# Kernel optimization log

Hardware: AMD Instinct MI355X
Metric: run time of the kernel (lower is better)

## Reference

```python
import jax, jax.numpy as jnp
import numpy as np

B, L, DIM = 4, 2048, 512
H, D = 8, 64
SCALE = D ** -0.5
NEG = -10000.0


def setup_inputs() -> dict:
    key = jax.random.key(0)
    ks = jax.random.split(key, 5)
    std = 1.0 / np.sqrt(DIM)
    return {
        "x": jax.random.normal(ks[0], (B, L, DIM), dtype=jnp.float32),
        "wq": jax.random.normal(ks[1], (H * D, DIM), dtype=jnp.float32) * std,
        "wk": jax.random.normal(ks[2], (H * D, DIM), dtype=jnp.float32) * std,
        "wv": jax.random.normal(ks[3], (H * D, DIM), dtype=jnp.float32) * std,
        "wo": jax.random.normal(ks[4], (DIM, H * D), dtype=jnp.float32) * std,
    }


def reference(x, wq, wk, wv, wo):
    b, l, _ = x.shape
    # projections (torch Linear: y = x @ W.T), split heads -> [b,h,l,d]
    q = (x @ wq.T).reshape(b, l, H, D).transpose(0, 2, 1, 3)
    k = (x @ wk.T).reshape(b, l, H, D).transpose(0, 2, 1, 3)
    v = (x @ wv.T).reshape(b, l, H, D).transpose(0, 2, 1, 3)
    scores = jnp.einsum("bhld,bhsd->bhls", q, k) * SCALE
    scores = jnp.nan_to_num(scores, nan=0.0, posinf=10000.0, neginf=NEG)
    diag = jnp.eye(l, dtype=bool)[None, None]  # [1,1,l,l]
    scores = jnp.where(diag, NEG, scores)
    attn = jax.nn.softmax(scores, axis=-1)
    attn = jnp.where(diag, 0.0, attn)
    attn = jnp.nan_to_num(attn, nan=0.0, posinf=0.0, neginf=0.0)
    out = jnp.einsum("bhls,bhsd->bhld", attn, v)
    out = out.transpose(0, 2, 1, 3).reshape(b, l, H * D)
    return out @ wo.T
```

## Files before the change

### kernel.cpp

```cpp
#include <hip/hip_runtime.h>
#include <hip/hip_bf16.h>


#define Bsz 4
#define Lsz 2048
#define DIMsz 512
#define Hsz 8
#define Dsz 64

typedef _Float16 f16;
typedef __attribute__((ext_vector_type(8))) _Float16 f16x8;
typedef __attribute__((ext_vector_type(4))) _Float16 f16x4;
typedef __attribute__((ext_vector_type(2))) __fp16 fp16x2;
typedef __attribute__((ext_vector_type(4))) float f32x4;
typedef __attribute__((ext_vector_type(16))) float f32x16;
typedef unsigned int u32;
typedef __attribute__((ext_vector_type(2))) unsigned int u32x2;

#if __has_builtin(__builtin_amdgcn_exp2f)
#define EXP2(x) __builtin_amdgcn_exp2f(x)
#else
#define EXP2(x) __expf(0.6931471805599453f * (x))
#endif

__device__ __forceinline__ u32 pack2(float a, float b) {
#if __has_builtin(__builtin_amdgcn_cvt_pkrtz)
    fp16x2 h = __builtin_amdgcn_cvt_pkrtz(a, b);
    return __builtin_bit_cast(u32, h);
#else
    fp16x2 h; h.x = (__fp16)a; h.y = (__fp16)b;
    return __builtin_bit_cast(u32, h);
#endif
}

#if __has_builtin(__builtin_amdgcn_permlane32_swap)
__device__ __forceinline__ void plswap(u32& a, u32& b) {
    u32x2 r = __builtin_amdgcn_permlane32_swap(a, b, false, false);
    a = r.x; b = r.y;
}
#else
__device__ __forceinline__ void plswap(u32& a, u32& b) {
    u32 sa = (u32)__shfl_xor((int)a, 32);
    u32 sb = (u32)__shfl_xor((int)b, 32);
    bool hi = (threadIdx.x & 32) != 0;
    u32 na = hi ? sb : a;
    u32 nb = hi ? b : sa;
    a = na; b = nb;
}
#endif

__device__ __forceinline__ void gl2lds16(const void* g, void* l) {
    __builtin_amdgcn_global_load_lds(
        (const __attribute__((address_space(1))) u32*)g,
        (__attribute__((address_space(3))) u32*)l, 16, 0, 0);
}

__global__ __launch_bounds__(256) void pack_f16(
    const float* __restrict__ x, const float* __restrict__ wq,
    const float* __restrict__ wk, const float* __restrict__ wv,
    const float* __restrict__ wo,
    f16* __restrict__ xh, f16* __restrict__ w3h, f16* __restrict__ woh)
{
    int bx = blockIdx.x, seg, blk;
    if (bx < 4096) { seg = 0; blk = bx; }
    else { seg = 1 + ((bx - 4096) >> 8); blk = (bx - 4096) & 255; }
    const float* s; f16* d; float sc = 1.0f;
    switch (seg) {
        case 0: s = x;  d = xh;            break;
        case 1: s = wq; d = w3h;           sc = 0.18033688011112042f; break;
        case 2: s = wk; d = w3h + 262144;  break;
        case 3: s = wv; d = w3h + 524288;  break;
        default: s = wo; d = woh;          break;
    }
    int i = (blk * 256 + threadIdx.x) * 4;
    float4 v = *(const float4*)(s + i);
    f16x4 o;
    o.x = (f16)(v.x * sc); o.y = (f16)(v.y * sc);
    o.z = (f16)(v.z * sc); o.w = (f16)(v.w * sc);
    *(f16x4*)(d + i) = o;
}

__global__ __launch_bounds__(256) void gemm_qkv_f16(
    const f16* __restrict__ A, const f16* __restrict__ B,
    f16* __restrict__ qh, f16* __restrict__ kh, f16* __restrict__ vth)
{
    __shared__ __align__(16) char smem[32768];
    f16* Ash = (f16*)smem;
    f16* Bsh = (f16*)(smem + 16384);

    const int tid = threadIdx.x;
    const int w = tid >> 6, lane = tid & 63;
    const int quad = lane >> 4, low = lane & 15;
    const int wm = w >> 1, wn = w & 1;
    const int m0 = blockIdx.y * 128, n0 = blockIdx.x * 128;

    f32x4 acc[4][4];
    #pragma unroll
    for (int i = 0; i < 4; i++)
        #pragma unroll
        for (int j = 0; j < 4; j++) acc[i][j] = (f32x4){0.f, 0.f, 0.f, 0.f};

    #pragma unroll 1
    for (int k0 = 0; k0 < DIMsz; k0 += 64) {
        __syncthreads();
        #pragma unroll
        for (int j = 0; j < 4; j++) {
            int t = j * 256 + tid;
            int r = t >> 3, g = t & 7;
            int gc = (g ^ (r & 7)) * 8;
            char* lb = (char*)Ash + (j * 256 + w * 64) * 16;
            gl2lds16(A + (size_t)(m0 + r) * DIMsz + k0 + gc, lb);
            char* lb2 = (char*)Bsh + (j * 256 + w * 64) * 16;
            gl2lds16(B + (size_t)(n0 + r) * DIMsz + k0 + gc, lb2);
        }
        __syncthreads();

        #pragma unroll
        for (int ks2 = 0; ks2 < 2; ks2++) {
            f16x8 af[4], bf[4];
            #pragma unroll
            for (int mt = 0; mt < 4; mt++) {
                int ar = wm * 64 + mt * 16 + low;
                int c = ks2 * 4 + quad;
                af[mt] = *(const f16x8*)&Ash[ar * 64 + ((c ^ (ar & 7)) << 3)];
            }
            #pragma unroll
            for (int nt = 0; nt < 4; nt++) {
                int br = wn * 64 + nt * 16 + low;
                int c = ks2 * 4 + quad;
                bf[nt] = *(const f16x8*)&Bsh[br * 64 + ((c ^ (br & 7)) << 3)];
            }
            #pragma unroll
            for (int mt = 0; mt < 4; mt++)
                #pragma unroll
                for (int nt = 0; nt < 4; nt++)
                    acc[mt][nt] = __builtin_amdgcn_mfma_f32_16x16x32_f16(
                        af[mt], bf[nt], acc[mt][nt], 0, 0, 0);
        }
    }

    const int proj = n0 >> 9;
    if (proj < 2) {
        f16* dst = (proj == 0) ? qh : kh;
        #pragma unroll
        for (int nt = 0; nt < 4; nt++) {
            int n = n0 + wn * 64 + nt * 16 + low;
            int c = n & 511, h = c >> 6, d = c & 63;
            #pragma unroll
            for (int mt = 0; mt < 4; mt++)
                #pragma unroll
                for (int r = 0; r < 4; r++) {
                    int m = m0 + wm * 64 + mt * 16 + quad * 4 + r;
                    int b_ = m >> 11, l = m & (Lsz - 1);
                    size_t bh = (size_t)(b_ * Hsz + h);
                    dst[(bh * Lsz + l) * Dsz + d] = (f16)acc[mt][nt][r];
                }
        }
    } else {
        const int hb = (n0 & 511) >> 6;
        f16* Tv = (f16*)smem;
        const int b_ = m0 >> 11, l0 = m0 & (Lsz - 1);
        #pragma unroll 1
        for (int hs = 0; hs < 2; hs++) {
            __syncthreads();
            if (wn == hs) {
                #pragma unroll
                for (int nt = 0; nt < 4; nt++) {
                    int d = nt * 16 + low;
                    #pragma unroll
                    for (int mt = 0; mt < 4; mt++)
                        #pragma unroll
                        for (int r = 0; r < 4; r++) {
                            int l = wm * 64 + mt * 16 + quad * 4 + r;
                            Tv[d * 136 + l] = (f16)acc[mt][nt][r];
                        }
                }
            }
            __syncthreads();
            int d = tid >> 2, seg = tid & 3;
            size_t bh = (size_t)(b_ * Hsz + hb + hs);
            f16* dstp = vth + (bh * 64 + d) * (size_t)Lsz + l0 + seg * 32;
            const f16* srcp = Tv + d * 136 + seg * 32;
            #pragma unroll
            for (int j = 0; j < 4; j++)
                *(f16x8*)(dstp + j * 8) = *(const f16x8*)(srcp + j * 8);
        }
    }
}

__global__ __launch_bounds__(256, 4) void attn_mfma(
    const f16* __restrict__ q, const f16* __restrict__ k,
    const f16* __restrict__ vt, f16* __restrict__ ctx)
{
    __shared__ __align__(16) char smem[33792];

    const int tid = threadIdx.x;
    const int w = tid >> 6, lane = tid & 63;
    const int col = lane & 31;
    const int h = lane >> 5;
    const int kw = w & 1, qw = w >> 1;
    const int bh = blockIdx.x;
    const int qb = blockIdx.y;
    const int q0 = qb * 64;
    const size_t kvb = (size_t)bh * Lsz;

    f16* Ks = (f16*)smem;
    f16* Vs = (f16*)(smem + 16384);

    f16x8 qf[4];
    #pragma unroll
    for (int s = 0; s < 4; s++)
        qf[s] = *(const f16x8*)(q + (kvb + q0 + qw * 32 + col) * Dsz
                                  + s * 16 + h * 8);
    #pragma unroll
    for (int s = 0; s < 4; s++)
        asm volatile("" :: "v"(qf[s]));

    const f16* kp; const f16* vp;
    {
        int r8 = tid >> 3, g8 = tid & 7;
        int gc = (g8 ^ (r8 & 7) ^ ((r8 >> 3) & 3)) << 3;
        kp = k + (kvb + r8) * Dsz + gc;
        vp = vt + ((size_t)bh * Dsz + r8) * Lsz + gc;
    }
    char* kl = (char*)smem + w * 1024;
    char* vl = (char*)smem + 16384 + w * 1024;

    const int cswz = (col & 7) ^ ((col >> 3) & 3);
    const f16* kfp[4];
    #pragma unroll
    for (int s = 0; s < 4; s++)
        kfp[s] = Ks + (kw * 32 + col) * 64 + (((s * 2 + h) ^ cswz) << 3);
    const f16* vfp[2][2];
    #pragma unroll
    for (int dt = 0; dt < 2; dt++)
        #pragma unroll
        for (int ks = 0; ks < 2; ks++) {
            int cv = kw * 4 + ks * 2 + h;
            vfp[dt][ks] = Vs + (dt * 32 + col) * 64 + ((cv ^ cswz) << 3);
        }

    f32x16 acc[2];
    #pragma unroll
    for (int dt = 0; dt < 2; dt++)
        #pragma unroll
        for (int i = 0; i < 16; i++) acc[dt][i] = 0.f;
    float lsum = 0.f;

    gl2lds16(kp,            kl);
    gl2lds16(kp + 32 * Dsz, kl + 4096);
    gl2lds16(vp,            vl);
    gl2lds16(vp + 32 * Lsz, vl + 4096);
    kp += 64 * Dsz;
    vp += 64;

#define ATTN_ROUND(S0, P, PRE) do {                                           \
    const int ko_ = (P) * 8192;                                               \
    if (PRE) {                                                                \
        const int nx_ = ((P) ^ 1) * 8192;                                     \
        gl2lds16(kp,            kl + nx_);                                    \
        gl2lds16(kp + 32 * Dsz, kl + nx_ + 4096);                             \
        gl2lds16(vp,            vl + nx_);                                    \
        gl2lds16(vp + 32 * Lsz, vl + nx_ + 4096);                             \
        kp += 64 * Dsz;                                                       \
        vp += 64;                                                             \
        asm volatile("s_waitcnt vmcnt(4)" ::: "memory");                      \
    } else {                                                                  \
        asm volatile("s_waitcnt vmcnt(0)" ::: "memory");                      \
    }                                                                         \
    __builtin_amdgcn_s_barrier();                                             \
    __builtin_amdgcn_sched_barrier(0);                                        \
      \
    f32x16 st;                                                                \
    _Pragma("unroll")                                                         \
    for (int i = 0; i < 16; i++) st[i] = 0.f;                                 \
    __builtin_amdgcn_s_setprio(1);                                            \
    _Pragma("unroll")                                                         \
    for (int s = 0; s < 4; s++) {                                             \
        f16x8 kf = *(const f16x8*)((const char*)kfp[s] + ko_);                \
        st = __builtin_amdgcn_mfma_f32_32x32x16_f16(kf, qf[s], st, 0, 0, 0);  \
    }                                                                         \
    __builtin_amdgcn_s_setprio(0);                                            \
                \
    _Pragma("unroll")                                                         \
    for (int i = 0; i < 16; i++) st[i] = EXP2(st[i]);                         \
    if ((S0) == q0 && kw == qw) {                                             \
        _Pragma("unroll")                                                     \
        for (int i = 0; i < 16; i++) {                                        \
            int row = (i & 3) + 8 * (i >> 2) + 4 * h;                         \
            st[i] = (row == col) ? 0.f : st[i];                               \
        }                                                                     \
    }                                                                         \
    _Pragma("unroll")                                                         \
    for (int i = 0; i < 16; i++) lsum += st[i];                               \
                                                \
    u32 P2[8];                                                                \
    _Pragma("unroll")                                                         \
    for (int j = 0; j < 8; j++)                                               \
        P2[j] = pack2(st[2 * j], st[2 * j + 1]);                              \
    plswap(P2[0], P2[2]); plswap(P2[1], P2[3]);                               \
    plswap(P2[4], P2[6]); plswap(P2[5], P2[7]);                               \
    union { u32 u[4]; f16x8 v; } pfa, pfb;                                    \
    _Pragma("unroll")                                                         \
    for (int jj = 0; jj < 4; jj++) {                                          \
        pfa.u[jj] = P2[jj];                                                   \
        pfb.u[jj] = P2[4 + jj];                                               \
    }                                                                         \
                               \
    __builtin_amdgcn_s_setprio(1);                                            \
    _Pragma("unroll")                                                         \
    for (int dt = 0; dt < 2; dt++) {                                          \
        f16x8 vf0 = *(const f16x8*)((const char*)vfp[dt][0] + ko_);           \
        acc[dt] = __builtin_amdgcn_mfma_f32_32x32x16_f16(                     \
            vf0, pfa.v, acc[dt], 0, 0, 0);                                    \
        f16x8 vf1 = *(const f16x8*)((const char*)vfp[dt][1] + ko_);           \
        acc[dt] = __builtin_amdgcn_mfma_f32_32x32x16_f16(                     \
            vf1, pfb.v, acc[dt], 0, 0, 0);                                    \
    }                                                                         \
    __builtin_amdgcn_s_setprio(0);                                            \
    __builtin_amdgcn_sched_barrier(0);                                        \
    __builtin_amdgcn_s_barrier();                                             \
} while (0)

    #pragma unroll 1
    for (int s0 = 0; s0 < Lsz; s0 += 128) {
        ATTN_ROUND(s0, 0, true);
        ATTN_ROUND(s0 + 64, 1, (s0 + 128 < Lsz));
    }
#undef ATTN_ROUND

    __syncthreads();

    float* Lsp = (float*)(smem + 32768);
    lsum += __shfl_xor(lsum, 32);
    if (h == 0) Lsp[qw * 64 + kw * 32 + col] = lsum;

    float* Om = (float*)smem;
    if (kw == 1) {
        float* og = Om + qw * 2048;
        #pragma unroll
        for (int dt = 0; dt < 2; dt++)
            #pragma unroll
            for (int i = 0; i < 16; i++) {
                int row = (i & 3) + 8 * (i >> 2) + 4 * h;
                og[(dt * 32 + row) * 32 + col] = acc[dt][i];
            }
    }
    __syncthreads();
    if (kw == 0) {
        const float* og = Om + qw * 2048;
        #pragma unroll
        for (int dt = 0; dt < 2; dt++)
            #pragma unroll
            for (int i = 0; i < 16; i++) {
                int row = (i & 3) + 8 * (i >> 2) + 4 * h;
                acc[dt][i] += og[(dt * 32 + row) * 32 + col];
            }
        const int b = bh >> 3, hh = bh & 7;
        float ls = Lsp[qw * 64 + col] + Lsp[qw * 64 + 32 + col];
        const float inv = 1.0f / ls;
        f16* op = ctx + ((size_t)(b * Lsz + q0 + qw * 32 + col)) * DIMsz
                      + hh * 64;
        #pragma unroll
        for (int dt = 0; dt < 2; dt++)
            #pragma unroll
            for (int r4 = 0; r4 < 4; r4++) {
                f16x4 o;
                o.x = (f16)(acc[dt][4 * r4 + 0] * inv);
                o.y = (f16)(acc[dt][4 * r4 + 1] * inv);
                o.z = (f16)(acc[dt][4 * r4 + 2] * inv);
                o.w = (f16)(acc[dt][4 * r4 + 3] * inv);
                *(f16x4*)(op + dt * 32 + 8 * r4 + 4 * h) = o;
            }
    }
}

__global__ __launch_bounds__(256) void gemm_out_f16(
    const f16* __restrict__ A, const f16* __restrict__ B,
    float* __restrict__ C)
{
    __shared__ f16 Ash[64 * 64];
    __shared__ f16 Bsh[64 * 64];
    const int tid = threadIdx.x;
    const int w = tid >> 6, lane = tid & 63;
    const int quad = lane >> 4, low = lane & 15;
    const int wm = w >> 1, wn = w & 1;
    const int m0 = blockIdx.y * 64, n0 = blockIdx.x * 64;

    f32x4 acc[2][2];
    #pragma unroll
    for (int i = 0; i < 2; i++)
        #pragma unroll
        for (int j = 0; j < 2; j++) acc[i][j] = (f32x4){0.f, 0.f, 0.f, 0.f};

    #pragma unroll 1
    for (int k0 = 0; k0 < DIMsz; k0 += 64) {
        __syncthreads();
        #pragma unroll
        for (int j = 0; j < 2; j++) {
            int t = j * 256 + tid;
            int r = t >> 3, g = t & 7;
            int gc = (g ^ (r & 7)) * 8;
            char* lb = (char*)Ash + (j * 256 + w * 64) * 16;
            gl2lds16(A + (size_t)(m0 + r) * DIMsz + k0 + gc, lb);
            char* lb2 = (char*)Bsh + (j * 256 + w * 64) * 16;
            gl2lds16(B + (size_t)(n0 + r) * DIMsz + k0 + gc, lb2);
        }
        __syncthreads();

        #pragma unroll
        for (int ks2 = 0; ks2 < 2; ks2++) {
            f16x8 af[2], bf[2];
            #pragma unroll
            for (int mt = 0; mt < 2; mt++) {
                int ar = wm * 32 + mt * 16 + low;
                int c = ks2 * 4 + quad;
                af[mt] = *(const f16x8*)&Ash[ar * 64 + ((c ^ (ar & 7)) << 3)];
            }
            #pragma unroll
            for (int nt = 0; nt < 2; nt++) {
                int br = wn * 32 + nt * 16 + low;
                int c = ks2 * 4 + quad;
                bf[nt] = *(const f16x8*)&Bsh[br * 64 + ((c ^ (br & 7)) << 3)];
            }
            #pragma unroll
            for (int mt = 0; mt < 2; mt++)
                #pragma unroll
                for (int nt = 0; nt < 2; nt++)
                    acc[mt][nt] = __builtin_amdgcn_mfma_f32_16x16x32_f16(
                        af[mt], bf[nt], acc[mt][nt], 0, 0, 0);
        }
    }

    #pragma unroll
    for (int mt = 0; mt < 2; mt++)
        #pragma unroll
        for (int r = 0; r < 4; r++) {
            int m = m0 + wm * 32 + mt * 16 + quad * 4 + r;
            #pragma unroll
            for (int nt = 0; nt < 2; nt++) {
                int n = n0 + wn * 32 + nt * 16 + low;
                C[(size_t)m * DIMsz + n] = acc[mt][nt][r];
            }
        }
}

extern "C" void kernel_launch(void* const* d_in, const int* in_sizes, int n_in,
                              void* d_out, int out_size, void* d_ws, size_t ws_size,
                              hipStream_t stream) {
    const float* x  = (const float*)d_in[0];
    const float* wq = (const float*)d_in[1];
    const float* wk = (const float*)d_in[2];
    const float* wv = (const float*)d_in[3];
    const float* wo = (const float*)d_in[4];
    float* out = (float*)d_out;

    const size_t NTOK = (size_t)Bsz * Lsz;
    const size_t XSZ  = NTOK * DIMsz;

    f16* xh   = (f16*)d_ws;
    f16* w3h  = xh + XSZ;
    f16* woh  = w3h + 3 * 262144;
    f16* qh   = woh + 262144;
    f16* kh   = qh + XSZ;
    f16* vth  = kh + XSZ;
    f16* ctxh = vth + XSZ;

    pack_f16<<<5120, 256, 0, stream>>>(x, wq, wk, wv, wo, xh, w3h, woh);

    dim3 g1(1536 / 128, NTOK / 128);
    gemm_qkv_f16<<<g1, 256, 0, stream>>>(xh, w3h, qh, kh, vth);

    dim3 g2(Bsz * Hsz, Lsz / 64);
    attn_mfma<<<g2, 256, 0, stream>>>(qh, kh, vth, ctxh);

    dim3 g3(DIMsz / 64, NTOK / 64);
    gemm_out_f16<<<g3, 256, 0, stream>>>(ctxh, woh, out);
}
```

Measured before the change: 161.2 us.

## Triple-buffer K/V tiles to drop trailing barrier; sum P via fdot2

```diff
diff --git a/kernel.cpp b/kernel.cpp
--- a/kernel.cpp
+++ b/kernel.cpp
@@ -188,11 +188,11 @@
     }
 }
 
-__global__ __launch_bounds__(256, 4) void attn_mfma(
+__global__ __launch_bounds__(256, 3) void attn_mfma(
     const f16* __restrict__ q, const f16* __restrict__ k,
     const f16* __restrict__ vt, f16* __restrict__ ctx)
 {
-    __shared__ __align__(16) char smem[33792];
+    __shared__ __align__(16) char smem[49664];
 
     const int tid = threadIdx.x;
     const int w = tid >> 6, lane = tid & 63;
@@ -205,7 +205,7 @@
     const size_t kvb = (size_t)bh * Lsz;
 
     f16* Ks = (f16*)smem;
-    f16* Vs = (f16*)(smem + 16384);
+    f16* Vs = (f16*)(smem + 24576);
 
     f16x8 qf[4];
     #pragma unroll
@@ -224,7 +224,7 @@
         vp = vt + ((size_t)bh * Dsz + r8) * Lsz + gc;
     }
     char* kl = (char*)smem + w * 1024;
-    char* vl = (char*)smem + 16384 + w * 1024;
+    char* vl = (char*)smem + 24576 + w * 1024;
 
     const int cswz = (col & 7) ^ ((col >> 3) & 3);
     const f16* kfp[4];
@@ -246,6 +246,10 @@
         #pragma unroll
         for (int i = 0; i < 16; i++) acc[dt][i] = 0.f;
     float lsum = 0.f;
+
+#if __has_builtin(__builtin_amdgcn_fdot2)
+    fp16x2 one2; one2.x = (__fp16)1.0f; one2.y = (__fp16)1.0f;
+#endif
 
     gl2lds16(kp,            kl);
     gl2lds16(kp + 32 * Dsz, kl + 4096);
@@ -254,84 +258,86 @@
     kp += 64 * Dsz;
     vp += 64;
 
-#define ATTN_ROUND(S0, P, PRE) do {                                           \
-    const int ko_ = (P) * 8192;                                               \
-    if (PRE) {                                                                \
-        const int nx_ = ((P) ^ 1) * 8192;                                     \
-        gl2lds16(kp,            kl + nx_);                                    \
-        gl2lds16(kp + 32 * Dsz, kl + nx_ + 4096);                             \
-        gl2lds16(vp,            vl + nx_);                                    \
-        gl2lds16(vp + 32 * Lsz, vl + nx_ + 4096);                             \
-        kp += 64 * Dsz;                                                       \
-        vp += 64;                                                             \
-        asm volatile("s_waitcnt vmcnt(4)" ::: "memory");                      \
-    } else {                                                                  \
-        asm volatile("s_waitcnt vmcnt(0)" ::: "memory");                      \
-    }                                                                         \
-    __builtin_amdgcn_s_barrier();                                             \
-    __builtin_amdgcn_sched_barrier(0);                                        \
-      \
-    f32x16 st;                                                                \
-    _Pragma("unroll")                                                         \
-    for (int i = 0; i < 16; i++) st[i] = 0.f;                                 \
-    __builtin_amdgcn_s_setprio(1);                                            \
-    _Pragma("unroll")                                                         \
-    for (int s = 0; s < 4; s++) {                                             \
-        f16x8 kf = *(const f16x8*)((const char*)kfp[s] + ko_);                \
-        st = __builtin_amdgcn_mfma_f32_32x32x16_f16(kf, qf[s], st, 0, 0, 0);  \
-    }                                                                         \
-    __builtin_amdgcn_s_setprio(0);                                            \
-                \
-    _Pragma("unroll")                                                         \
-    for (int i = 0; i < 16; i++) st[i] = EXP2(st[i]);                         \
-    if ((S0) == q0 && kw == qw) {                                             \
-        _Pragma("unroll")                                                     \
-        for (int i = 0; i < 16; i++) {                                        \
-            int row = (i & 3) + 8 * (i >> 2) + 4 * h;                         \
-            st[i] = (row == col) ? 0.f : st[i];                               \
-        }                                                                     \
-    }                                                                         \
-    _Pragma("unroll")                                                         \
-    for (int i = 0; i < 16; i++) lsum += st[i];                               \
-                                                \
-    u32 P2[8];                                                                \
-    _Pragma("unroll")                                                         \
-    for (int j = 0; j < 8; j++)                                               \
-        P2[j] = pack2(st[2 * j], st[2 * j + 1]);                              \
-    plswap(P2[0], P2[2]); plswap(P2[1], P2[3]);                               \
-    plswap(P2[4], P2[6]); plswap(P2[5], P2[7]);                               \
-    union { u32 u[4]; f16x8 v; } pfa, pfb;                                    \
-    _Pragma("unroll")                                                         \
-    for (int jj = 0; jj < 4; jj++) {                                          \
-        pfa.u[jj] = P2[jj];                                                   \
-        pfb.u[jj] = P2[4 + jj];                                               \
-    }                                                                         \
-                               \
-    __builtin_amdgcn_s_setprio(1);                                            \
-    _Pragma("unroll")                                                         \
-    for (int dt = 0; dt < 2; dt++) {                                          \
-        f16x8 vf0 = *(const f16x8*)((const char*)vfp[dt][0] + ko_);           \
-        acc[dt] = __builtin_amdgcn_mfma_f32_32x32x16_f16(                     \
-            vf0, pfa.v, acc[dt], 0, 0, 0);                                    \
-        f16x8 vf1 = *(const f16x8*)((const char*)vfp[dt][1] + ko_);           \
-        acc[dt] = __builtin_amdgcn_mfma_f32_32x32x16_f16(                     \
-            vf1, pfb.v, acc[dt], 0, 0, 0);                                    \
-    }                                                                         \
-    __builtin_amdgcn_s_setprio(0);                                            \
-    __builtin_amdgcn_sched_barrier(0);                                        \
-    __builtin_amdgcn_s_barrier();                                             \
-} while (0)
-
+    int off0 = 0, off1 = 8192, off2 = 16384;
     #pragma unroll 1
-    for (int s0 = 0; s0 < Lsz; s0 += 128) {
-        ATTN_ROUND(s0, 0, true);
-        ATTN_ROUND(s0 + 64, 1, (s0 + 128 < Lsz));
-    }
-#undef ATTN_ROUND
+    for (int r = 0; r < Lsz / 64; ++r) {
+        if (r < Lsz / 64 - 1) {
+            gl2lds16(kp,            kl + off1);
+            gl2lds16(kp + 32 * Dsz, kl + off1 + 4096);
+            gl2lds16(vp,            vl + off1);
+            gl2lds16(vp + 32 * Lsz, vl + off1 + 4096);
+            kp += 64 * Dsz;
+            vp += 64;
+            asm volatile("s_waitcnt vmcnt(4)" ::: "memory");
+        } else {
+            asm volatile("s_waitcnt vmcnt(0)" ::: "memory");
+        }
+        __builtin_amdgcn_s_barrier();
+        __builtin_amdgcn_sched_barrier(0);
+
+        f32x16 st;
+        #pragma unroll
+        for (int i = 0; i < 16; i++) st[i] = 0.f;
+        __builtin_amdgcn_s_setprio(1);
+        #pragma unroll
+        for (int s = 0; s < 4; s++) {
+            f16x8 kf = *(const f16x8*)((const char*)kfp[s] + off0);
+            st = __builtin_amdgcn_mfma_f32_32x32x16_f16(kf, qf[s], st, 0, 0, 0);
+        }
+        __builtin_amdgcn_s_setprio(0);
+
+        #pragma unroll
+        for (int i = 0; i < 16; i++) st[i] = EXP2(st[i]);
+        if (r == qb && kw == qw) {
+            #pragma unroll
+            for (int i = 0; i < 16; i++) {
+                int row = (i & 3) + 8 * (i >> 2) + 4 * h;
+                st[i] = (row == col) ? 0.f : st[i];
+            }
+        }
+
+        u32 P2[8];
+        #pragma unroll
+        for (int j = 0; j < 8; j++)
+            P2[j] = pack2(st[2 * j], st[2 * j + 1]);
+
+#if __has_builtin(__builtin_amdgcn_fdot2)
+        #pragma unroll
+        for (int j = 0; j < 8; j++)
+            lsum = __builtin_amdgcn_fdot2(
+                __builtin_bit_cast(fp16x2, P2[j]), one2, lsum, false);
+#else
+        #pragma unroll
+        for (int i = 0; i < 16; i++) lsum += st[i];
+#endif
+
+        plswap(P2[0], P2[2]); plswap(P2[1], P2[3]);
+        plswap(P2[4], P2[6]); plswap(P2[5], P2[7]);
+        union { u32 u[4]; f16x8 v; } pfa, pfb;
+        #pragma unroll
+        for (int jj = 0; jj < 4; jj++) {
+            pfa.u[jj] = P2[jj];
+            pfb.u[jj] = P2[4 + jj];
+        }
+
+        __builtin_amdgcn_s_setprio(1);
+        #pragma unroll
+        for (int dt = 0; dt < 2; dt++) {
+            f16x8 vf0 = *(const f16x8*)((const char*)vfp[dt][0] + off0);
+            acc[dt] = __builtin_amdgcn_mfma_f32_32x32x16_f16(
+                vf0, pfa.v, acc[dt], 0, 0, 0);
+            f16x8 vf1 = *(const f16x8*)((const char*)vfp[dt][1] + off0);
+            acc[dt] = __builtin_amdgcn_mfma_f32_32x32x16_f16(
+                vf1, pfb.v, acc[dt], 0, 0, 0);
+        }
+        __builtin_amdgcn_s_setprio(0);
+
+        int t_ = off0; off0 = off1; off1 = off2; off2 = t_;
+    }
 
     __syncthreads();
 
-    float* Lsp = (float*)(smem + 32768);
+    float* Lsp = (float*)(smem + 49152);
     lsum += __shfl_xor(lsum, 32);
     if (h == 0) Lsp[qw * 64 + kw * 32 + col] = lsum;
 
```

Result: slower. 165.5 us (+2.7%).

## Double attention query tile to 128 with 512-thread blocks and fdot2 row sums

Applied to the files above, without the earlier changes.

```diff
diff --git a/kernel.cpp b/kernel.cpp
--- a/kernel.cpp
+++ b/kernel.cpp
@@ -188,7 +188,7 @@
     }
 }
 
-__global__ __launch_bounds__(256, 4) void attn_mfma(
+__global__ __launch_bounds__(512, 8) void attn_mfma(
     const f16* __restrict__ q, const f16* __restrict__ k,
     const f16* __restrict__ vt, f16* __restrict__ ctx)
 {
@@ -201,7 +201,7 @@
     const int kw = w & 1, qw = w >> 1;
     const int bh = blockIdx.x;
     const int qb = blockIdx.y;
-    const int q0 = qb * 64;
+    const int q0 = qb * 128;
     const size_t kvb = (size_t)bh * Lsz;
 
     f16* Ks = (f16*)smem;
@@ -247,24 +247,27 @@
         for (int i = 0; i < 16; i++) acc[dt][i] = 0.f;
     float lsum = 0.f;
 
-    gl2lds16(kp,            kl);
-    gl2lds16(kp + 32 * Dsz, kl + 4096);
-    gl2lds16(vp,            vl);
-    gl2lds16(vp + 32 * Lsz, vl + 4096);
+#if __has_builtin(__builtin_amdgcn_fdot2)
+    fp16x2 one2; one2.x = (__fp16)1.0f; one2.y = (__fp16)1.0f;
+#endif
+
+    const int dpar = (qw - kw) & 1;
+    const int drnd = 2 * qb + ((qw - kw) >> 1);
+
+    gl2lds16(kp, kl);
+    gl2lds16(vp, vl);
     kp += 64 * Dsz;
     vp += 64;
 
-#define ATTN_ROUND(S0, P, PRE) do {                                           \
+#define ATTN_ROUND(R, P, PRE) do {                                            \
     const int ko_ = (P) * 8192;                                               \
     if (PRE) {                                                                \
         const int nx_ = ((P) ^ 1) * 8192;                                     \
-        gl2lds16(kp,            kl + nx_);                                    \
-        gl2lds16(kp + 32 * Dsz, kl + nx_ + 4096);                             \
-        gl2lds16(vp,            vl + nx_);                                    \
-        gl2lds16(vp + 32 * Lsz, vl + nx_ + 4096);                             \
+        gl2lds16(kp, kl + nx_);                                               \
+        gl2lds16(vp, vl + nx_);                                               \
         kp += 64 * Dsz;                                                       \
         vp += 64;                                                             \
-        asm volatile("s_waitcnt vmcnt(4)" ::: "memory");                      \
+        asm volatile("s_waitcnt vmcnt(2)" ::: "memory");                      \
     } else {                                                                  \
         asm volatile("s_waitcnt vmcnt(0)" ::: "memory");                      \
     }                                                                         \
@@ -284,20 +287,25 @@
                 \
     _Pragma("unroll")                                                         \
     for (int i = 0; i < 16; i++) st[i] = EXP2(st[i]);                         \
-    if ((S0) == q0 && kw == qw) {                                             \
+    if (dpar == 0 && (R) == drnd) {                                           \
         _Pragma("unroll")                                                     \
         for (int i = 0; i < 16; i++) {                                        \
             int row = (i & 3) + 8 * (i >> 2) + 4 * h;                         \
             st[i] = (row == col) ? 0.f : st[i];                               \
         }                                                                     \
     }                                                                         \
-    _Pragma("unroll")                                                         \
-    for (int i = 0; i < 16; i++) lsum += st[i];                               \
                                                 \
     u32 P2[8];                                                                \
     _Pragma("unroll")                                                         \
     for (int j = 0; j < 8; j++)                                               \
         P2[j] = pack2(st[2 * j], st[2 * j + 1]);                              \
+            \
+    _Pragma("unroll")                                                         \
+    for (int j = 0; j < 8; j++) {                                             \
+        IF_FDOT2(lsum = __builtin_amdgcn_fdot2(                               \
+            __builtin_bit_cast(fp16x2, P2[j]), one2, lsum, false);)           \
+        IF_NO_FDOT2(lsum += st[2 * j] + st[2 * j + 1];)                       \
+    }                                                                         \
     plswap(P2[0], P2[2]); plswap(P2[1], P2[3]);                               \
     plswap(P2[4], P2[6]); plswap(P2[5], P2[7]);                               \
     union { u32 u[4]; f16x8 v; } pfa, pfb;                                    \
@@ -322,12 +330,22 @@
     __builtin_amdgcn_s_barrier();                                             \
 } while (0)
 
+#if __has_builtin(__builtin_amdgcn_fdot2)
+#define IF_FDOT2(X) X
+#define IF_NO_FDOT2(X)
+#else
+#define IF_FDOT2(X)
+#define IF_NO_FDOT2(X) X
+#endif
+
     #pragma unroll 1
-    for (int s0 = 0; s0 < Lsz; s0 += 128) {
-        ATTN_ROUND(s0, 0, true);
-        ATTN_ROUND(s0 + 64, 1, (s0 + 128 < Lsz));
+    for (int r = 0; r < Lsz / 64; r += 2) {
+        ATTN_ROUND(r, 0, true);
+        ATTN_ROUND(r + 1, 1, (r + 2 < Lsz / 64));
     }
 #undef ATTN_ROUND
+#undef IF_FDOT2
+#undef IF_NO_FDOT2
 
     __syncthreads();
 
@@ -471,8 +489,8 @@
     dim3 g1(1536 / 128, NTOK / 128);
     gemm_qkv_f16<<<g1, 256, 0, stream>>>(xh, w3h, qh, kh, vth);
 
-    dim3 g2(Bsz * Hsz, Lsz / 64);
-    attn_mfma<<<g2, 256, 0, stream>>>(qh, kh, vth, ctxh);
+    dim3 g2(Bsz * Hsz, Lsz / 128);
+    attn_mfma<<<g2, 512, 0, stream>>>(qh, kh, vth, ctxh);
 
     dim3 g3(DIMsz / 64, NTOK / 64);
     gemm_out_f16<<<g3, 256, 0, stream>>>(ctxh, woh, out);
```

Result: slower. 252.7 us (+56.8%).
